# Optimization experiments

Measured on AMD Instinct MI355X. Metric: run time of the kernel, lower is better.

The kernel has to match this reference:

```python
import jax, jax.numpy as jnp
import numpy as np

EPS = 1e-8
NEG_FILL = -9e15


def _normalize(x):
    # matches torch cosine_similarity's norm clamp with eps=1e-8
    n = jnp.sqrt(jnp.sum(x * x, axis=-1, keepdims=True))
    return x / jnp.maximum(n, EPS)


def setup_inputs() -> dict:
    key = jax.random.key(0)
    k1, k2 = jax.random.split(key)
    N, D = 8192, 512
    cxr_feats = jax.random.normal(k1, (N, D), dtype=jnp.float32)
    ehr_feats = jax.random.normal(k2, (N, D), dtype=jnp.float32)
    temperature = jnp.asarray(0.07, dtype=jnp.float32)
    return {"cxr_feats": cxr_feats, "ehr_feats": ehr_feats, "temperature": temperature}


def reference(cxr_feats, ehr_feats, temperature):
    # normalize then GEMM instead of broadcasted [N,N,D] cosine_similarity
    cn = _normalize(cxr_feats)                      # [N, D]
    en = _normalize(ehr_feats)                      # [N, D]
    cos_sim = jnp.einsum('id,jd->ij', cn, en)       # [N, N]
    cos_sim = cos_sim / temperature
    N = cos_sim.shape[0]
    eye = jnp.eye(N, dtype=bool)
    diag = jnp.diagonal(cos_sim)                    # positives
    cos_neg = jnp.where(eye, NEG_FILL, cos_sim)     # mask self-pairs
    nll_1 = diag - jax.nn.logsumexp(cos_neg, axis=1)
    nll_2 = diag - jax.nn.logsumexp(cos_neg, axis=0)
    loss = -jnp.mean(nll_1 + nll_2)
    return loss
```

## Files before the change

### kernel.cpp

```cpp
#include <hip/hip_runtime.h>
#include <hip/hip_bf16.h>
#include <stdint.h>
#include <stddef.h>

#define NROWS 8192
#define DDIM  512
#define TILE  128
#define BKB   128
#define NBLK  (NROWS / TILE)

static_assert(NBLK == 64, "bj extraction assumes 64 col-blocks");

typedef float f32x4 __attribute__((ext_vector_type(4)));
typedef long  v2l  __attribute__((ext_vector_type(2)));

__device__ __forceinline__ void async_copy16(const void* g, void* l) {
    __builtin_amdgcn_global_load_lds(
        (const __attribute__((address_space(1))) uint32_t*)g,
        (__attribute__((address_space(3))) uint32_t*)l,
        16, 0, 0);
}

__global__ __launch_bounds__(256) void prep_kernel(
    const float* __restrict__ CXR, const float* __restrict__ EHR,
    uint32_t* __restrict__ CN8, uint32_t* __restrict__ EN8,
    float* __restrict__ rowsum ,
    float* __restrict__ out)
{
    if (blockIdx.x < 64) {
        rowsum[blockIdx.x * 256 + threadIdx.x] = 0.f;
        if (blockIdx.x == 0 && threadIdx.x == 0) out[0] = 0.f;
    }
    const int half = (blockIdx.x >= 2048);
    const float* X = half ? EHR : CXR;
    uint32_t* Y = half ? EN8 : CN8;
    const int row  = (blockIdx.x & 2047) * 4 + (threadIdx.x >> 6);
    const int lane = threadIdx.x & 63;
    const float* xr = X + (size_t)row * DDIM;
    float4 v0 = ((const float4*)xr)[lane];
    float4 v1 = ((const float4*)xr)[lane + 64];
    float ss = v0.x*v0.x + v0.y*v0.y + v0.z*v0.z + v0.w*v0.w
             + v1.x*v1.x + v1.y*v1.y + v1.z*v1.z + v1.w*v1.w;
    #pragma unroll
    for (int d = 1; d < 64; d <<= 1) ss += __shfl_xor(ss, d);
    const float sc = 1.0f / fmaxf(sqrtf(ss), 1e-8f);
    uint32_t* yr = Y + (size_t)row * (DDIM / 4);
    int w0 = __builtin_amdgcn_cvt_pk_fp8_f32(v0.x*sc, v0.y*sc, 0, false);
    w0     = __builtin_amdgcn_cvt_pk_fp8_f32(v0.z*sc, v0.w*sc, w0, true);
    int w1 = __builtin_amdgcn_cvt_pk_fp8_f32(v1.x*sc, v1.y*sc, 0, false);
    w1     = __builtin_amdgcn_cvt_pk_fp8_f32(v1.z*sc, v1.w*sc, w1, true);
    yr[lane]      = (uint32_t)w0;
    yr[lane + 64] = (uint32_t)w1;
}

__global__ __launch_bounds__(256, 4) void gemm_loss_kernel(
    const uint8_t* __restrict__ A,
    const uint8_t* __restrict__ B,
    const float* __restrict__ temp_p,
    float* __restrict__ rowsum,
    float* __restrict__ colsum,
    float* __restrict__ diagv)
{
    __shared__ uint8_t As[TILE * BKB];
    __shared__ uint8_t Bs[TILE * BKB];

    const int tid  = threadIdx.x;
    const int lane = tid & 63;
    const int wv   = tid >> 6;
    const int wi   = (wv >> 1) * 64;
    const int wj   = (wv & 1) * 64;
    const int lcol = lane & 15;
    const int q    = lane >> 4;

    const int bi = blockIdx.x & (NBLK - 1);
    const int bj = blockIdx.x >> 6;
    const int row0 = bi * TILE;
    const int col0 = bj * TILE;

    const int sr = lane >> 3;
    const int su = (lane & 7) ^ sr;
    const uint8_t* Ag = A + (size_t)(row0 + wv * 32 + sr) * DDIM + su * 16;
    const uint8_t* Bg = B + (size_t)(col0 + wv * 32 + sr) * DDIM + su * 16;

    f32x4 acc[4][4] = {};

    for (int k0 = 0; k0 < DDIM; k0 += BKB) {
        __syncthreads();
        #pragma unroll
        for (int c = 0; c < 4; ++c) {
            async_copy16(Ag + (size_t)(c * 8) * DDIM + k0, &As[(wv * 32 + c * 8) * BKB]);
            async_copy16(Bg + (size_t)(c * 8) * DDIM + k0, &Bs[(wv * 32 + c * 8) * BKB]);
        }
        __syncthreads();

        #pragma unroll
        for (int kk2 = 0; kk2 < 2; ++kk2) {
            const int u = kk2 * 4 + q;
            long aflo[4], afhi[4];
            #pragma unroll
            for (int mt = 0; mt < 4; ++mt) {
                const int r = wi + mt * 16 + lcol;
                v2l a16 = *(const v2l*)&As[r * BKB + (u ^ (r & 7)) * 16];
                aflo[mt] = a16.x; afhi[mt] = a16.y;
            }
            #pragma unroll
            for (int nt = 0; nt < 4; ++nt) {
                const int r = wj + nt * 16 + lcol;
                v2l b16 = *(const v2l*)&Bs[r * BKB + (u ^ (r & 7)) * 16];
                #pragma unroll
                for (int mt = 0; mt < 4; ++mt)
                    acc[mt][nt] = __builtin_amdgcn_mfma_f32_16x16x32_fp8_fp8(
                        aflo[mt], b16.x, acc[mt][nt], 0, 0, 0);
                #pragma unroll
                for (int mt = 0; mt < 4; ++mt)
                    acc[mt][nt] = __builtin_amdgcn_mfma_f32_16x16x32_fp8_fp8(
                        afhi[mt], b16.y, acc[mt][nt], 0, 0, 0);
            }
        }
    }

    const float invT = 1.0f / temp_p[0];
    const float M = invT;

    float rs[4][4];
    float cs[4];
    #pragma unroll
    for (int mt = 0; mt < 4; ++mt)
        #pragma unroll
        for (int r = 0; r < 4; ++r) rs[mt][r] = 0.f;
    #pragma unroll
    for (int nt = 0; nt < 4; ++nt) cs[nt] = 0.f;

    #pragma unroll
    for (int mt = 0; mt < 4; ++mt) {
        #pragma unroll
        for (int nt = 0; nt < 4; ++nt) {
            #pragma unroll
            for (int r = 0; r < 4; ++r) {
                const int gi = row0 + wi + mt * 16 + q * 4 + r;
                const int gj = col0 + wj + nt * 16 + lcol;
                const float sv = acc[mt][nt][r] * invT;
                float e;
                if (gi == gj) { diagv[gi] = sv; e = 0.f; }
                else          { e = __expf(sv - M); }
                rs[mt][r] += e;
                cs[nt]    += e;
            }
        }
    }

    #pragma unroll
    for (int d = 1; d < 16; d <<= 1)
        #pragma unroll
        for (int mt = 0; mt < 4; ++mt)
            #pragma unroll
            for (int r = 0; r < 4; ++r)
                rs[mt][r] += __shfl_xor(rs[mt][r], d);

    #pragma unroll
    for (int d = 16; d < 64; d <<= 1)
        #pragma unroll
        for (int nt = 0; nt < 4; ++nt)
            cs[nt] += __shfl_xor(cs[nt], d);

    if (lcol == 0) {
        #pragma unroll
        for (int mt = 0; mt < 4; ++mt)
            #pragma unroll
            for (int r = 0; r < 4; ++r)
                atomicAdd(&rowsum[row0 + wi + mt * 16 + q * 4 + r], rs[mt][r]);
    }
    if (q == 0) {
        #pragma unroll
        for (int nt = 0; nt < 4; ++nt)
            atomicAdd(&colsum[col0 + wj + nt * 16 + lcol], cs[nt]);
    }
}

__global__ __launch_bounds__(256) void finalize_kernel(
    const float* __restrict__ rowsum, const float* __restrict__ colsum,
    const float* __restrict__ diagv,  const float* __restrict__ temp_p,
    float* __restrict__ out)
{
    __shared__ float red[4];
    const float M = 1.0f / temp_p[0];
    const int i = blockIdx.x * 256 + threadIdx.x;
    float s = 2.f * M + logf(rowsum[i]) + logf(colsum[i]) - 2.f * diagv[i];
    #pragma unroll
    for (int d = 1; d < 64; d <<= 1) s += __shfl_xor(s, d);
    if ((threadIdx.x & 63) == 0) red[threadIdx.x >> 6] = s;
    __syncthreads();
    if (threadIdx.x == 0)
        atomicAdd(out, (red[0] + red[1] + red[2] + red[3]) / (float)NROWS);
}

extern "C" void kernel_launch(void* const* d_in, const int* in_sizes, int n_in,
                              void* d_out, int out_size, void* d_ws, size_t ws_size,
                              hipStream_t stream) {
    (void)in_sizes; (void)n_in; (void)out_size; (void)ws_size;
    const float* cxr    = (const float*)d_in[0];
    const float* ehr    = (const float*)d_in[1];
    const float* temp_p = (const float*)d_in[2];
    float* out = (float*)d_out;

    float* rowsum = (float*)d_ws;
    float* colsum = rowsum + NROWS;
    float* diagv  = colsum + NROWS;
    uint32_t* cn8 = (uint32_t*)(diagv + NROWS);
    uint32_t* en8 = cn8 + (size_t)NROWS * (DDIM / 4);
    const uint8_t* cnb = (const uint8_t*)cn8;
    const uint8_t* enb = (const uint8_t*)en8;

    prep_kernel<<<4096, 256, 0, stream>>>(cxr, ehr, cn8, en8, rowsum, out);
    gemm_loss_kernel<<<NBLK * NBLK, 256, 0, stream>>>(cnb, enb, temp_p, rowsum, colsum, diagv);
    finalize_kernel<<<NROWS / 256, 256, 0, stream>>>(rowsum, colsum, diagv, temp_p, out);
}
```

Measured before the change: 134.6 us.

## Use scaled 16x16x128 FP8 MFMA and exp2-based epilogue in GEMM-loss kernel

Replaces the 16x16x32 FP8 MFMA sequence with the MI355X scaled 16x16x128 f8f6f4 MFMA, using unit scales (0x7F exponent). Each lane now loads two 16-byte K-chunks per operand into a 256-bit fragment, and the K tile is covered with one quarter as many MFMA instructions. The epilogue folds the temperature and log2e into a single fma feeding the native exp2 instead of multiply, subtract and __expf. The occupancy hint drops from 4 to 3 waves per SIMD to leave room for the wider fragment registers, which may reduce latency hiding.

After: 379.4 us. 2.82x slower.

```diff
diff --git a/kernel.cpp b/kernel.cpp
--- a/kernel.cpp
+++ b/kernel.cpp
@@ -12,7 +12,8 @@
 static_assert(NBLK == 64, "bj extraction assumes 64 col-blocks");
 
 typedef float f32x4 __attribute__((ext_vector_type(4)));
-typedef long  v2l  __attribute__((ext_vector_type(2)));
+typedef int   i32x4 __attribute__((ext_vector_type(4)));
+typedef int   i32x8 __attribute__((ext_vector_type(8)));
 
 __device__ __forceinline__ void async_copy16(const void* g, void* l) {
     __builtin_amdgcn_global_load_lds(
@@ -53,7 +54,7 @@
     yr[lane + 64] = (uint32_t)w1;
 }
 
-__global__ __launch_bounds__(256, 4) void gemm_loss_kernel(
+__global__ __launch_bounds__(256, 3) void gemm_loss_kernel(
     const uint8_t* __restrict__ A,
     const uint8_t* __restrict__ B,
     const float* __restrict__ temp_p,
@@ -71,6 +72,7 @@
     const int wj   = (wv & 1) * 64;
     const int lcol = lane & 15;
     const int q    = lane >> 4;
+    const int u0   = q << 1;
 
     const int bi = blockIdx.x & (NBLK - 1);
     const int bj = blockIdx.x >> 6;
@@ -83,6 +85,7 @@
     const uint8_t* Bg = B + (size_t)(col0 + wv * 32 + sr) * DDIM + su * 16;
 
     f32x4 acc[4][4] = {};
+    const int SC1 = 0x7F7F7F7F;
 
     for (int k0 = 0; k0 < DDIM; k0 += BKB) {
         __syncthreads();
@@ -93,34 +96,33 @@
         }
         __syncthreads();
 
-        #pragma unroll
-        for (int kk2 = 0; kk2 < 2; ++kk2) {
-            const int u = kk2 * 4 + q;
-            long aflo[4], afhi[4];
-            #pragma unroll
-            for (int mt = 0; mt < 4; ++mt) {
-                const int r = wi + mt * 16 + lcol;
-                v2l a16 = *(const v2l*)&As[r * BKB + (u ^ (r & 7)) * 16];
-                aflo[mt] = a16.x; afhi[mt] = a16.y;
-            }
-            #pragma unroll
-            for (int nt = 0; nt < 4; ++nt) {
-                const int r = wj + nt * 16 + lcol;
-                v2l b16 = *(const v2l*)&Bs[r * BKB + (u ^ (r & 7)) * 16];
-                #pragma unroll
-                for (int mt = 0; mt < 4; ++mt)
-                    acc[mt][nt] = __builtin_amdgcn_mfma_f32_16x16x32_fp8_fp8(
-                        aflo[mt], b16.x, acc[mt][nt], 0, 0, 0);
-                #pragma unroll
-                for (int mt = 0; mt < 4; ++mt)
-                    acc[mt][nt] = __builtin_amdgcn_mfma_f32_16x16x32_fp8_fp8(
-                        afhi[mt], b16.y, acc[mt][nt], 0, 0, 0);
-            }
+        i32x8 af[4];
+        #pragma unroll
+        for (int mt = 0; mt < 4; ++mt) {
+            const int r = wi + mt * 16 + lcol;
+            const uint8_t* base = &As[r * BKB];
+            i32x4 lo = *(const i32x4*)&base[((u0    ) ^ (r & 7)) * 16];
+            i32x4 hi = *(const i32x4*)&base[((u0 + 1) ^ (r & 7)) * 16];
+            af[mt] = __builtin_shufflevector(lo, hi, 0, 1, 2, 3, 4, 5, 6, 7);
+        }
+        #pragma unroll
+        for (int nt = 0; nt < 4; ++nt) {
+            const int r = wj + nt * 16 + lcol;
+            const uint8_t* base = &Bs[r * BKB];
+            i32x4 lo = *(const i32x4*)&base[((u0    ) ^ (r & 7)) * 16];
+            i32x4 hi = *(const i32x4*)&base[((u0 + 1) ^ (r & 7)) * 16];
+            i32x8 bf = __builtin_shufflevector(lo, hi, 0, 1, 2, 3, 4, 5, 6, 7);
+            #pragma unroll
+            for (int mt = 0; mt < 4; ++mt)
+                acc[mt][nt] = __builtin_amdgcn_mfma_scale_f32_16x16x128_f8f6f4(
+                    af[mt], bf, acc[mt][nt],
+                    0 , 0 ,
+                    0, SC1, 0, SC1);
         }
     }
 
     const float invT = 1.0f / temp_p[0];
-    const float M = invT;
+    const float c2   = invT * 1.442695040888963f;
 
     float rs[4][4];
     float cs[4];
@@ -139,10 +141,10 @@
             for (int r = 0; r < 4; ++r) {
                 const int gi = row0 + wi + mt * 16 + q * 4 + r;
                 const int gj = col0 + wj + nt * 16 + lcol;
-                const float sv = acc[mt][nt][r] * invT;
+                const float a = acc[mt][nt][r];
                 float e;
-                if (gi == gj) { diagv[gi] = sv; e = 0.f; }
-                else          { e = __expf(sv - M); }
+                if (gi == gj) { diagv[gi] = a * invT; e = 0.f; }
+                else          { e = __builtin_amdgcn_exp2f(fmaf(a, c2, -c2)); }
                 rs[mt][r] += e;
                 cs[nt]    += e;
             }
```

## Double-buffer LDS tiles in fp8 GEMM and use exp2 with fused scale

Applied to the files above, without the earlier changes.

Splits the shared-memory A/B tiles into two buffers so the async global-to-LDS copy for the next K chunk is issued while MFMAs run on the current one, with one barrier per iteration instead of two. The launch-bounds occupancy hint drops from 4 to 2 blocks because LDS use doubles to 64KB per block. The epilogue also replaces expf(sv*invT - invT) with a native exp2 of an FMA on a prescaled constant, saving a multiply and the expf range handling. The cost is lower occupancy and higher register pressure in exchange for overlapping loads with compute.

Result: slower. 163.9 us (+21.8%).

```diff
diff --git a/kernel.cpp b/kernel.cpp
--- a/kernel.cpp
+++ b/kernel.cpp
@@ -53,7 +53,7 @@
     yr[lane + 64] = (uint32_t)w1;
 }
 
-__global__ __launch_bounds__(256, 4) void gemm_loss_kernel(
+__global__ __launch_bounds__(256, 2) void gemm_loss_kernel(
     const uint8_t* __restrict__ A,
     const uint8_t* __restrict__ B,
     const float* __restrict__ temp_p,
@@ -61,8 +61,8 @@
     float* __restrict__ colsum,
     float* __restrict__ diagv)
 {
-    __shared__ uint8_t As[TILE * BKB];
-    __shared__ uint8_t Bs[TILE * BKB];
+    __shared__ uint8_t As[2][TILE * BKB];
+    __shared__ uint8_t Bs[2][TILE * BKB];
 
     const int tid  = threadIdx.x;
     const int lane = tid & 63;
@@ -84,14 +84,21 @@
 
     f32x4 acc[4][4] = {};
 
-    for (int k0 = 0; k0 < DDIM; k0 += BKB) {
-        __syncthreads();
+    auto stage = [&](int buf, int k0) {
         #pragma unroll
         for (int c = 0; c < 4; ++c) {
-            async_copy16(Ag + (size_t)(c * 8) * DDIM + k0, &As[(wv * 32 + c * 8) * BKB]);
-            async_copy16(Bg + (size_t)(c * 8) * DDIM + k0, &Bs[(wv * 32 + c * 8) * BKB]);
+            async_copy16(Ag + (size_t)(c * 8) * DDIM + k0, &As[buf][(wv * 32 + c * 8) * BKB]);
+            async_copy16(Bg + (size_t)(c * 8) * DDIM + k0, &Bs[buf][(wv * 32 + c * 8) * BKB]);
         }
-        __syncthreads();
+    };
+
+    stage(0, 0);
+    __syncthreads();
+
+    #pragma unroll
+    for (int t = 0; t < 4; ++t) {
+        const int cur = t & 1;
+        if (t < 3) stage(cur ^ 1, (t + 1) * BKB);
 
         #pragma unroll
         for (int kk2 = 0; kk2 < 2; ++kk2) {
@@ -100,13 +107,13 @@
             #pragma unroll
             for (int mt = 0; mt < 4; ++mt) {
                 const int r = wi + mt * 16 + lcol;
-                v2l a16 = *(const v2l*)&As[r * BKB + (u ^ (r & 7)) * 16];
+                v2l a16 = *(const v2l*)&As[cur][r * BKB + (u ^ (r & 7)) * 16];
                 aflo[mt] = a16.x; afhi[mt] = a16.y;
             }
             #pragma unroll
             for (int nt = 0; nt < 4; ++nt) {
                 const int r = wj + nt * 16 + lcol;
-                v2l b16 = *(const v2l*)&Bs[r * BKB + (u ^ (r & 7)) * 16];
+                v2l b16 = *(const v2l*)&Bs[cur][r * BKB + (u ^ (r & 7)) * 16];
                 #pragma unroll
                 for (int mt = 0; mt < 4; ++mt)
                     acc[mt][nt] = __builtin_amdgcn_mfma_f32_16x16x32_fp8_fp8(
@@ -117,10 +124,12 @@
                         afhi[mt], b16.y, acc[mt][nt], 0, 0, 0);
             }
         }
+
+        if (t < 3) __syncthreads();
     }
 
     const float invT = 1.0f / temp_p[0];
-    const float M = invT;
+    const float c2   = invT * 1.442695040888963f;
 
     float rs[4][4];
     float cs[4];
@@ -139,10 +148,10 @@
             for (int r = 0; r < 4; ++r) {
                 const int gi = row0 + wi + mt * 16 + q * 4 + r;
                 const int gj = col0 + wj + nt * 16 + lcol;
-                const float sv = acc[mt][nt][r] * invT;
+                const float a = acc[mt][nt][r];
                 float e;
-                if (gi == gj) { diagv[gi] = sv; e = 0.f; }
-                else          { e = __expf(sv - M); }
+                if (gi == gj) { diagv[gi] = a * invT; e = 0.f; }
+                else          { e = __builtin_amdgcn_exp2f(fmaf(a, c2, -c2)); }
                 rs[mt][r] += e;
                 cs[nt]    += e;
             }
```
